# Performance work log

Measured on AMD Instinct MI355X. Metric: run time of the kernel, lower is better.

The kernel has to match this reference:

```python
import jax, jax.numpy as jnp
import numpy as np
from jax import lax

POOL_K, POOL_S, FINAL, KNN = 5, 3, 6, 819  # pool size/stride, adaptive out, k_neighbors


def setup_inputs() -> dict:
    key = jax.random.key(0)
    k1, k2, k3 = jax.random.split(key, 3)
    return {
        "x": jax.random.normal(k1, (64, 3, 32, 32), jnp.float32),
        "conv_weight": jax.random.normal(k2, (2048, 3, 6, 6), jnp.float32) * 0.05,
        "conv_bias": jax.random.normal(k3, (1, 2048, 1, 1), jnp.float32),
    }


def lowestk_heaviside(x, k):
    # indicator of the k channel-wise smallest values: x < (k+1)-th smallest
    kth = jnp.sort(x, axis=1)[:, k:k + 1]  # [B,1,H,W]
    return (x < kth).astype(x.dtype)


def avg_pool_ceil(x, k, s):
    # torch avg_pool2d(ceil_mode=True, padding=0): partial windows clipped to
    # the input and divided by the number of valid elements.
    H, W = x.shape[2], x.shape[3]
    oh = -(-(H - k) // s) + 1
    ow = -(-(W - k) // s) + 1
    ph = max(0, (oh - 1) * s + k - H)
    pw = max(0, (ow - 1) * s + k - W)
    dims, strides = (1, 1, k, k), (1, 1, s, s)
    pad = ((0, 0), (0, 0), (0, ph), (0, pw))
    sums = lax.reduce_window(x, 0.0, lax.add, dims, strides, pad)
    cnt = lax.reduce_window(jnp.ones((1, 1, H, W), x.dtype), 0.0, lax.add,
                            dims, strides, pad)
    return sums / cnt


def adaptive_avg_pool2d(x, n):
    # torch adaptive bins: [floor(i*S/n), ceil((i+1)*S/n)); separable in H/W
    def pool_axis(y, axis):
        size = y.shape[axis]
        parts = []
        for i in range(n):
            s = (i * size) // n
            e = -(-((i + 1) * size) // n)
            parts.append(lax.slice_in_dim(y, s, e, axis=axis)
                         .mean(axis=axis, keepdims=True))
        return jnp.concatenate(parts, axis=axis)
    return pool_axis(pool_axis(x, 2), 3)


def reference(x, conv_weight, conv_bias):
    out = lax.conv_general_dilated(x, conv_weight, (1, 1), 'VALID',
                                   dimension_numbers=('NCHW', 'OIHW', 'NCHW'))

    def branch(z):
        m = lowestk_heaviside(z, KNN)            # [B,2048,27,27]
        m = avg_pool_ceil(m, POOL_K, POOL_S)     # [B,2048,9,9]
        return adaptive_avg_pool2d(m, FINAL)     # [B,2048,6,6]

    out1 = branch(-out + conv_bias)
    out2 = branch(out + conv_bias)
    return (out1, out2)
```

## Files before the change

kernel.cpp:

```cpp
#include <hip/hip_runtime.h>
#include <cstdint>
#include <cstddef>

#define RANK_K 819

__device__ __forceinline__ int zbin256(float z) {
  float t = (z + 8.0f) * 16.0f;
  t = t < 0.0f ? 0.0f : (t > 255.0f ? 255.0f : t);
  return (int)t;
}

__global__ __launch_bounds__(256) void net99_wtrans(const float* __restrict__ w,
                                                    float* __restrict__ wt) {
  int idx = blockIdx.x * 256 + threadIdx.x;
  if (idx < 2048 * 108) {
    int kk = idx / 2048, c = idx % 2048;
    int ic = kk % 3, sp = kk / 3, ky = sp / 6, kx = sp % 6;
    wt[idx] = w[c * 108 + ic * 36 + ky * 6 + kx];
  }
}

__global__ __launch_bounds__(256) void net99_conv(const float* __restrict__ x,
                                                  const float* __restrict__ wt,
                                                  float* __restrict__ conv, int b0) {
  const int y  = blockIdx.x;
  const int ct = blockIdx.y;
  const int bl = blockIdx.z;
  const int b  = b0 + bl;
  const int tid = threadIdx.x;
  __shared__ float xs[3][6][32];
  for (int i = tid; i < 576; i += 256) {
    int ic = i / 192, rem = i % 192, r = rem / 32, col = rem % 32;
    xs[ic][r][col] = x[((b * 3 + ic) * 32 + (y + r)) * 32 + col];
  }
  __syncthreads();
  const int c = ct * 256 + tid;
  const float* wtc = wt + c;
  float acc[27];
#pragma unroll
  for (int q = 0; q < 27; ++q) acc[q] = 0.0f;
  for (int ky = 0; ky < 6; ++ky) {
    float xd[3][32];
#pragma unroll
    for (int i = 0; i < 96; ++i) {
      int ic = i >> 5, col = i & 31;
      xd[ic][col] = xs[ic][ky][col];
    }
#pragma unroll
    for (int kx = 0; kx < 6; ++kx) {
#pragma unroll
      for (int ic = 0; ic < 3; ++ic) {
        float wv = wtc[(size_t)((ky * 6 + kx) * 3 + ic) * 2048];
#pragma unroll
        for (int q = 0; q < 27; ++q)
          acc[q] = fmaf(wv, xd[ic][kx + q], acc[q]);
      }
    }
  }
  float* dst = conv + ((size_t)(bl * 27 + y) * 27) * 2048 + c;
#pragma unroll
  for (int q = 0; q < 27; ++q) dst[(size_t)q * 2048] = acc[q];
}

__global__ __launch_bounds__(256) void net99_select(const float* __restrict__ conv,
                                                    const float* __restrict__ bias,
                                                    uint8_t* __restrict__ mskb, int b0) {
  const int bl = blockIdx.x / 365;
  const int g  = blockIdx.x % 365;
  const int p0 = 2 * g;
  const bool has1 = (p0 + 1) < 729;
  const int gb = b0 + bl;
  const int tid  = threadIdx.x;
  const int lane = tid & 63;
  const int wid  = tid >> 6;
  const int nst  = has1 ? 4 : 2;
  __shared__ uint32_t hist[4][256];
  __shared__ float    cand[4][512];
  __shared__ int      cnt[4];
  __shared__ int      sbin[4], sbelow[4];
  __shared__ float    skth[4];

  const float4* __restrict__ s0 =
      (const float4*)(conv + ((size_t)bl * 729 + p0) * 2048) + tid * 2;
  const float4* __restrict__ b4 = (const float4*)bias + tid * 2;
  float4 va0 = s0[0], vb0 = s0[1];
  float4 va1 = {}, vb1 = {};
  if (has1) { va1 = s0[512]; vb1 = s0[513]; }
  float4 ba = b4[0], bb = b4[1];

  (&hist[0][0])[tid]       = 0u;
  (&hist[0][0])[tid + 256] = 0u;
  (&hist[0][0])[tid + 512] = 0u;
  (&hist[0][0])[tid + 768] = 0u;
  if (tid < 4) cnt[tid] = 0;

  float z[4][8];
  {
    float bv[8] = {ba.x, ba.y, ba.z, ba.w, bb.x, bb.y, bb.z, bb.w};
    float v0[8] = {va0.x, va0.y, va0.z, va0.w, vb0.x, vb0.y, vb0.z, vb0.w};
    float v1[8] = {va1.x, va1.y, va1.z, va1.w, vb1.x, vb1.y, vb1.z, vb1.w};
#pragma unroll
    for (int j = 0; j < 8; ++j) {
      z[0][j] = bv[j] - v0[j];
      z[1][j] = bv[j] + v0[j];
      z[2][j] = bv[j] - v1[j];
      z[3][j] = bv[j] + v1[j];
    }
  }
  __syncthreads();
#pragma unroll
  for (int j = 0; j < 8; ++j) {
    atomicAdd(&hist[0][zbin256(z[0][j])], 1u);
    atomicAdd(&hist[1][zbin256(z[1][j])], 1u);
  }
  if (has1) {
#pragma unroll
    for (int j = 0; j < 8; ++j) {
      atomicAdd(&hist[2][zbin256(z[2][j])], 1u);
      atomicAdd(&hist[3][zbin256(z[3][j])], 1u);
    }
  }
  __syncthreads();
  if (wid < nst) {
    const int s = wid;
    int h[4];
#pragma unroll
    for (int t = 0; t < 4; ++t) h[t] = (int)hist[s][lane * 4 + t];
    int loc = h[0] + h[1] + h[2] + h[3];
    int inc = loc;
#pragma unroll
    for (int off = 1; off < 64; off <<= 1) {
      int u = __shfl_up(inc, off);
      if (lane >= off) inc += u;
    }
    int pre = inc - loc;
    if (pre <= RANK_K && RANK_K < pre + loc) {
      int cum = pre;
#pragma unroll
      for (int t = 0; t < 4; ++t) {
        if (RANK_K < cum + h[t]) { sbin[s] = lane * 4 + t; sbelow[s] = cum; break; }
        cum += h[t];
      }
    }
  }
  __syncthreads();
#pragma unroll
  for (int s = 0; s < 4; ++s) {
    if (s >= 2 && !has1) break;
    const int tb = sbin[s];
#pragma unroll
    for (int j = 0; j < 8; ++j) {
      if (zbin256(z[s][j]) == tb) {
        int u = atomicAdd(&cnt[s], 1);
        if (u < 512) cand[s][u] = z[s][j];
      }
    }
  }
  __syncthreads();
  if (wid < nst) {
    const int s = wid;
    int cN = cnt[s] < 512 ? cnt[s] : 512;
    int rloc = RANK_K - sbelow[s];
    for (int ci = lane; ci < cN; ci += 64) {
      float v = cand[s][ci]; int rk = 0;
      for (int j = 0; j < cN; ++j) {
        float u = cand[s][j];
        rk += (u < v) || (u == v && j < ci);
      }
      if (rk == rloc) skth[s] = v;
    }
  }
  __syncthreads();
  const size_t pix0 = (size_t)gb * 729 + p0;
  {
    uint32_t m0 = 0u, m1 = 0u;
    const float k0 = skth[0], k1 = skth[1];
#pragma unroll
    for (int j = 0; j < 8; ++j) {
      m0 |= (uint32_t)(z[0][j] < k0) << j;
      m1 |= (uint32_t)(z[1][j] < k1) << j;
    }
    mskb[pix0 * 256 + tid]                        = (uint8_t)m0;
    mskb[((size_t)64 * 729 + pix0) * 256 + tid]   = (uint8_t)m1;
  }
  if (has1) {
    uint32_t m2 = 0u, m3 = 0u;
    const float k2 = skth[2], k3 = skth[3];
#pragma unroll
    for (int j = 0; j < 8; ++j) {
      m2 |= (uint32_t)(z[2][j] < k2) << j;
      m3 |= (uint32_t)(z[3][j] < k3) << j;
    }
    mskb[(pix0 + 1) * 256 + tid]                      = (uint8_t)m2;
    mskb[((size_t)64 * 729 + pix0 + 1) * 256 + tid]   = (uint8_t)m3;
  }
}

__global__ __launch_bounds__(256) void net99_pool(const uint32_t* __restrict__ msk,
                                                  float* __restrict__ out) {
  __shared__ uint32_t stage[729 * 8];
  const int blk = blockIdx.x;
  const int cg  = blk & 7;
  const int sb  = blk >> 3;
  const int tid = threadIdx.x;
  const uint32_t* src = msk + (size_t)sb * 729 * 64 + cg * 8;
  for (int i = tid; i < 729 * 8; i += 256) {
    int p = i >> 3, w = i & 7;
    stage[i] = src[(size_t)p * 64 + w];
  }
  __syncthreads();
  const int lw = tid >> 5, sel = tid & 31;
  uint32_t rbm[27];
  for (int y = 0; y < 27; ++y) {
    uint32_t rb = 0;
#pragma unroll
    for (int xx = 0; xx < 27; ++xx)
      rb |= ((stage[(y * 27 + xx) * 8 + lw] >> sel) & 1u) << xx;
    rbm[y] = rb;
  }
  constexpr uint32_t WM[9] = {0x1Fu, 0xF8u, 0x7C0u, 0x3E00u, 0x1F000u,
                              0xF8000u, 0x7C0000u, 0x3E00000u, 0x7000000u};
  constexpr int CC[9]  = {5, 5, 5, 5, 5, 5, 5, 5, 3};
  constexpr int BW0[6] = {0, 1, 3, 4, 6, 7};
  constexpr int BW1[6] = {1, 2, 4, 5, 7, 8};
  const int s = sb >> 6, b = sb & 63, c = cg * 256 + tid;
  float* dst = out + (size_t)s * 4718592 + (size_t)(b * 2048 + c) * 36;
  for (int i = 0; i < 6; ++i) {
    float P[2][9];
#pragma unroll
    for (int t = 0; t < 2; ++t) {
      int r  = t ? BW1[i] : BW0[i];
      int y0 = 3 * r;
      int y1 = (y0 + 5 > 27) ? 27 : y0 + 5;
      int cr = y1 - y0;
      int pp[9];
#pragma unroll
      for (int cx = 0; cx < 9; ++cx) pp[cx] = 0;
      for (int yy = y0; yy < y1; ++yy) {
        uint32_t rb = rbm[yy];
#pragma unroll
        for (int cx = 0; cx < 9; ++cx) pp[cx] += __popc(rb & WM[cx]);
      }
#pragma unroll
      for (int cx = 0; cx < 9; ++cx)
        P[t][cx] = (float)pp[cx] / (float)(cr * CC[cx]);
    }
    float M[9];
#pragma unroll
    for (int cx = 0; cx < 9; ++cx) M[cx] = (P[0][cx] + P[1][cx]) * 0.5f;
#pragma unroll
    for (int j = 0; j < 6; ++j)
      dst[i * 6 + j] = (M[BW0[j]] + M[BW1[j]]) * 0.5f;
  }
}

extern "C" void kernel_launch(void* const* d_in, const int* in_sizes, int n_in,
                              void* d_out, int out_size, void* d_ws, size_t ws_size,
                              hipStream_t stream) {
  const float* x    = (const float*)d_in[0];
  const float* w    = (const float*)d_in[1];
  const float* bias = (const float*)d_in[2];
  float* out = (float*)d_out;
  uint8_t* ws = (uint8_t*)d_ws;

  const size_t WT_BYTES   = (size_t)108 * 2048 * 4;
  const size_t MASK_OFF   = WT_BYTES;
  const size_t MASK_BYTES = (size_t)2 * 64 * 729 * 64 * 4;
  const size_t CONV_OFF   = MASK_OFF + MASK_BYTES;
  const size_t PER_B      = (size_t)2048 * 729 * 4;

  float*    wt   = (float*)ws;
  uint8_t*  mskb = (uint8_t*)(ws + MASK_OFF);
  uint32_t* msk  = (uint32_t*)(ws + MASK_OFF);
  float*    conv = (float*)(ws + CONV_OFF);

  size_t avail = ws_size > CONV_OFF ? ws_size - CONV_OFF : 0;
  int Bc = (int)(avail / PER_B);
  if (Bc < 1) Bc = 1;
  if (Bc > 64) Bc = 64;

  hipLaunchKernelGGL(net99_wtrans, dim3((2048 * 108 + 255) / 256), dim3(256), 0, stream, w, wt);
  for (int b0 = 0; b0 < 64; b0 += Bc) {
    int nb = (64 - b0 < Bc) ? (64 - b0) : Bc;
    hipLaunchKernelGGL(net99_conv, dim3(27, 8, nb), dim3(256), 0, stream, x, wt, conv, b0);
    hipLaunchKernelGGL(net99_select, dim3(nb * 365), dim3(256), 0, stream, conv, bias, mskb, b0);
  }
  hipLaunchKernelGGL(net99_pool, dim3(1024), dim3(256), 0, stream, msk, out);
}
```

Baseline: 493.5 us.

## Rewrite conv with packed FP32 FMAs, scalar-loaded inputs and split output rows

The convolution kernel now computes two output channels per thread (c and c+1024) using v_pk_fma_f32, with one input operand taken from scalar registers. Input rows are loaded with s_load_dwordx16/x4 instead of being staged in shared memory. Each block covers 14 output columns instead of 27 (halves overlap by one column), which cuts accumulator register pressure, and launch bounds now request 4 blocks per CU. The weight transpose writes interleaved channel pairs to match. This aims to double FMA throughput and raise occupancy, at the cost of inline-asm fragility and some duplicated work on the overlapping column.

```diff
diff --git a/kernel.cpp b/kernel.cpp
--- a/kernel.cpp
+++ b/kernel.cpp
@@ -3,6 +3,23 @@
 #include <cstddef>
 
 #define RANK_K 819
+
+typedef __attribute__((ext_vector_type(2)))  float f32x2;
+typedef __attribute__((ext_vector_type(4)))  float f32x4s;
+typedef __attribute__((ext_vector_type(16))) float f32x16;
+
+__device__ __forceinline__ f32x2 pk_fma_blo(f32x2 a, f32x2 bs, f32x2 c) {
+  f32x2 d;
+  asm("v_pk_fma_f32 %0, %1, %2, %3 op_sel_hi:[1,0,1]"
+      : "=v"(d) : "v"(a), "s"(bs), "v"(c));
+  return d;
+}
+__device__ __forceinline__ f32x2 pk_fma_bhi(f32x2 a, f32x2 bs, f32x2 c) {
+  f32x2 d;
+  asm("v_pk_fma_f32 %0, %1, %2, %3 op_sel:[0,1,0] op_sel_hi:[1,1,1]"
+      : "=v"(d) : "v"(a), "s"(bs), "v"(c));
+  return d;
+}
 
 __device__ __forceinline__ int zbin256(float z) {
   float t = (z + 8.0f) * 16.0f;
@@ -11,55 +28,98 @@
 }
 
 __global__ __launch_bounds__(256) void net99_wtrans(const float* __restrict__ w,
-                                                    float* __restrict__ wt) {
+                                                    f32x2* __restrict__ wt4) {
   int idx = blockIdx.x * 256 + threadIdx.x;
-  if (idx < 2048 * 108) {
-    int kk = idx / 2048, c = idx % 2048;
-    int ic = kk % 3, sp = kk / 3, ky = sp / 6, kx = sp % 6;
-    wt[idx] = w[c * 108 + ic * 36 + ky * 6 + kx];
-  }
-}
-
-__global__ __launch_bounds__(256) void net99_conv(const float* __restrict__ x,
-                                                  const float* __restrict__ wt,
-                                                  float* __restrict__ conv, int b0) {
-  const int y  = blockIdx.x;
-  const int ct = blockIdx.y;
-  const int bl = blockIdx.z;
-  const int b  = b0 + bl;
+  if (idx < 108 * 1024) {
+    int k = idx / 1024, cc = idx % 1024;
+    int ic = k % 3, sp = k / 3, ky = sp / 6, kx = sp % 6;
+    int wo = ic * 36 + ky * 6 + kx;
+    f32x2 t;
+    t.x = w[cc * 108 + wo];
+    t.y = w[(cc + 1024) * 108 + wo];
+    wt4[idx] = t;
+  }
+}
+
+__global__ __launch_bounds__(256, 4) void net99_conv(const float* __restrict__ x,
+                                                     const f32x2* __restrict__ wt4,
+                                                     float* __restrict__ conv, int b0) {
+  const int y   = blockIdx.x;
+  const int ctq = blockIdx.y;
+  const int ct  = ctq & 3;
+  const int qh  = ctq >> 2;
+  const int bl  = blockIdx.z;
+  const int b   = b0 + bl;
   const int tid = threadIdx.x;
-  __shared__ float xs[3][6][32];
-  for (int i = tid; i < 576; i += 256) {
-    int ic = i / 192, rem = i % 192, r = rem / 32, col = rem % 32;
-    xs[ic][r][col] = x[((b * 3 + ic) * 32 + (y + r)) * 32 + col];
-  }
-  __syncthreads();
-  const int c = ct * 256 + tid;
-  const float* wtc = wt + c;
-  float acc[27];
-#pragma unroll
-  for (int q = 0; q < 27; ++q) acc[q] = 0.0f;
+  const int q0  = 13 * qh;
+  const int cpair = ct * 256 + tid;
+  const f32x2* wtc = wt4 + cpair;
+  f32x2 acc[14];
+#pragma unroll
+  for (int q = 0; q < 14; ++q) acc[q] = (f32x2)(0.0f);
+#pragma unroll 1
   for (int ky = 0; ky < 6; ++ky) {
-    float xd[3][32];
-#pragma unroll
-    for (int i = 0; i < 96; ++i) {
-      int ic = i >> 5, col = i & 31;
-      xd[ic][col] = xs[ic][ky][col];
-    }
-#pragma unroll
-    for (int kx = 0; kx < 6; ++kx) {
-#pragma unroll
-      for (int ic = 0; ic < 3; ++ic) {
-        float wv = wtc[(size_t)((ky * 6 + kx) * 3 + ic) * 2048];
-#pragma unroll
-        for (int q = 0; q < 27; ++q)
-          acc[q] = fmaf(wv, xd[ic][kx + q], acc[q]);
-      }
-    }
-  }
-  float* dst = conv + ((size_t)(bl * 27 + y) * 27) * 2048 + c;
-#pragma unroll
-  for (int q = 0; q < 27; ++q) dst[(size_t)q * 2048] = acc[q];
+    const float* r0 = x + ((b * 3 + 0) * 32 + (y + ky)) * 32 + q0;
+    const float* r1 = x + ((b * 3 + 1) * 32 + (y + ky)) * 32 + q0;
+    const float* r2 = x + ((b * 3 + 2) * 32 + (y + ky)) * 32 + q0;
+    f32x2 wv[6][3];
+#pragma unroll
+    for (int kx = 0; kx < 6; ++kx)
+#pragma unroll
+      for (int ic = 0; ic < 3; ++ic)
+        wv[kx][ic] = wtc[(size_t)((ky * 6 + kx) * 3 + ic) * 1024];
+    f32x16 a0, a1, a2; f32x4s e0, e1, e2;
+    asm volatile(
+        "s_load_dwordx16 %0, %6, 0x0\n\t"
+        "s_load_dwordx16 %1, %7, 0x0\n\t"
+        "s_load_dwordx16 %2, %8, 0x0\n\t"
+        "s_load_dwordx4  %3, %6, 0x40\n\t"
+        "s_load_dwordx4  %4, %7, 0x40\n\t"
+        "s_load_dwordx4  %5, %8, 0x40\n\t"
+        "s_waitcnt lgkmcnt(0)"
+        : "=&s"(a0), "=&s"(a1), "=&s"(a2), "=&s"(e0), "=&s"(e1), "=&s"(e2)
+        : "s"(r0), "s"(r1), "s"(r2));
+    __builtin_amdgcn_sched_barrier(0);
+#pragma unroll
+    for (int r = 0; r < 19; ++r) {
+      f32x2 p0, p1, p2;
+      if (r < 16) {
+        p0.x = a0[(r >> 1) * 2]; p0.y = a0[(r >> 1) * 2 + 1];
+        p1.x = a1[(r >> 1) * 2]; p1.y = a1[(r >> 1) * 2 + 1];
+        p2.x = a2[(r >> 1) * 2]; p2.y = a2[(r >> 1) * 2 + 1];
+      } else {
+        const int rr = r - 16;
+        p0.x = e0[(rr >> 1) * 2]; p0.y = e0[(rr >> 1) * 2 + 1];
+        p1.x = e1[(rr >> 1) * 2]; p1.y = e1[(rr >> 1) * 2 + 1];
+        p2.x = e2[(rr >> 1) * 2]; p2.y = e2[(rr >> 1) * 2 + 1];
+      }
+#pragma unroll
+      for (int kx = 0; kx < 6; ++kx) {
+        const int qi = r - kx;
+        if (qi >= 0 && qi < 14) {
+          if (r & 1) {
+            acc[qi] = pk_fma_bhi(wv[kx][0], p0, acc[qi]);
+            acc[qi] = pk_fma_bhi(wv[kx][1], p1, acc[qi]);
+            acc[qi] = pk_fma_bhi(wv[kx][2], p2, acc[qi]);
+          } else {
+            acc[qi] = pk_fma_blo(wv[kx][0], p0, acc[qi]);
+            acc[qi] = pk_fma_blo(wv[kx][1], p1, acc[qi]);
+            acc[qi] = pk_fma_blo(wv[kx][2], p2, acc[qi]);
+          }
+        }
+      }
+    }
+  }
+  float* dstbase = conv + ((size_t)(bl * 27 + y) * 27) * 2048;
+  const int qstart = qh;
+#pragma unroll
+  for (int qi = 0; qi < 14; ++qi) {
+    if (qi >= qstart) {
+      const int q = q0 + qi;
+      dstbase[(size_t)q * 2048 + cpair]        = acc[qi].x;
+      dstbase[(size_t)q * 2048 + cpair + 1024] = acc[qi].y;
+    }
+  }
 }
 
 __global__ __launch_bounds__(256) void net99_select(const float* __restrict__ conv,
@@ -180,8 +240,8 @@
       m0 |= (uint32_t)(z[0][j] < k0) << j;
       m1 |= (uint32_t)(z[1][j] < k1) << j;
     }
-    mskb[pix0 * 256 + tid]                        = (uint8_t)m0;
-    mskb[((size_t)64 * 729 + pix0) * 256 + tid]   = (uint8_t)m1;
+    mskb[pix0 * 256 + tid]                      = (uint8_t)m0;
+    mskb[((size_t)64 * 729 + pix0) * 256 + tid] = (uint8_t)m1;
   }
   if (has1) {
     uint32_t m2 = 0u, m3 = 0u;
@@ -263,13 +323,13 @@
   float* out = (float*)d_out;
   uint8_t* ws = (uint8_t*)d_ws;
 
-  const size_t WT_BYTES   = (size_t)108 * 2048 * 4;
+  const size_t WT_BYTES   = (size_t)108 * 1024 * 8;
   const size_t MASK_OFF   = WT_BYTES;
   const size_t MASK_BYTES = (size_t)2 * 64 * 729 * 64 * 4;
   const size_t CONV_OFF   = MASK_OFF + MASK_BYTES;
   const size_t PER_B      = (size_t)2048 * 729 * 4;
 
-  float*    wt   = (float*)ws;
+  f32x2*    wt4  = (f32x2*)ws;
   uint8_t*  mskb = (uint8_t*)(ws + MASK_OFF);
   uint32_t* msk  = (uint32_t*)(ws + MASK_OFF);
   float*    conv = (float*)(ws + CONV_OFF);
@@ -279,10 +339,10 @@
   if (Bc < 1) Bc = 1;
   if (Bc > 64) Bc = 64;
 
-  hipLaunchKernelGGL(net99_wtrans, dim3((2048 * 108 + 255) / 256), dim3(256), 0, stream, w, wt);
+  hipLaunchKernelGGL(net99_wtrans, dim3((108 * 1024 + 255) / 256), dim3(256), 0, stream, w, wt4);
   for (int b0 = 0; b0 < 64; b0 += Bc) {
     int nb = (64 - b0 < Bc) ? (64 - b0) : Bc;
-    hipLaunchKernelGGL(net99_conv, dim3(27, 8, nb), dim3(256), 0, stream, x, wt, conv, b0);
+    hipLaunchKernelGGL(net99_conv, dim3(27, 8, nb), dim3(256), 0, stream, x, wt4, conv, b0);
     hipLaunchKernelGGL(net99_select, dim3(nb * 365), dim3(256), 0, stream, conv, bias, mskb, b0);
   }
   hipLaunchKernelGGL(net99_pool, dim3(1024), dim3(256), 0, stream, msk, out);
```

Result: faster. 460.1 us (-6.8%).
